# Performance work log

Hardware: AMD Instinct MI355X
Metric: run time of the kernel (lower is better)

The kernel has to match this reference:

```python
import jax, jax.numpy as jnp
import numpy as np

B, L, D, H, TOPK = 64, 1024, 16, 128, 64
SCALE = H ** -0.5  # proj_dim ** -0.5


def _linear_params(k, fan_in, fan_out):
    W = jax.random.normal(k, (fan_in, fan_out), jnp.float32) / np.sqrt(fan_in).astype(np.float32)
    b = jnp.zeros((fan_out,), jnp.float32)
    return W, b


def setup_inputs() -> dict:
    key = jax.random.key(0)
    ks = jax.random.split(key, 9)
    x = jax.random.normal(ks[0], (B, L, D), jnp.float32)
    Wq, bq = _linear_params(ks[1], D, H)
    Wk, bk = _linear_params(ks[2], D, H)
    phi_W1, phi_b1 = _linear_params(ks[3], D, H)
    phi_W2, phi_b2 = _linear_params(ks[4], H, H)
    xi_W1, xi_b1 = _linear_params(ks[5], 2 * D, H)
    xi_W2, xi_b2 = _linear_params(ks[6], H, H)
    rho_W1, rho_b1 = _linear_params(ks[7], H, H)
    rho_W2, rho_b2 = _linear_params(ks[8], H, H)
    return {
        "x": x,
        "Wq": Wq, "bq": bq, "Wk": Wk, "bk": bk,
        "phi_W1": phi_W1, "phi_b1": phi_b1, "phi_W2": phi_W2, "phi_b2": phi_b2,
        "xi_W1": xi_W1, "xi_b1": xi_b1, "xi_W2": xi_W2, "xi_b2": xi_b2,
        "rho_W1": rho_W1, "rho_b1": rho_b1, "rho_W2": rho_W2, "rho_b2": rho_b2,
    }


def _gather_rows(x, idx):
    # x: (B, L, D), idx: (B, K) -> (B, K, D)
    return jnp.take_along_axis(x, jnp.broadcast_to(idx[:, :, None], idx.shape + (x.shape[-1],)), axis=1)


def reference(x, Wq, bq, Wk, bk,
              phi_W1, phi_b1, phi_W2, phi_b2,
              xi_W1, xi_b1, xi_W2, xi_b2,
              rho_W1, rho_b1, rho_W2, rho_b2):
    # padding mask (trim is identity for dense random inputs; mask is all-True)
    mask = jnp.abs(x).sum(-1) != 0  # (B, L)
    Q = x @ Wq + bq                 # (B, L, H)
    K = x @ Wk + bk                 # (B, L, H)
    scores = jnp.einsum("blh,bmh->blm", Q, K) * SCALE  # (B, L, L)
    mask_2d = mask[:, :, None] & mask[:, None, :]
    scores = jnp.where(mask_2d, scores, -jnp.inf)
    flat = scores.reshape(B, L * L)
    topk_vals, topk_idx = jax.lax.top_k(flat, TOPK)    # (B, K)
    topk_w = jax.nn.softmax(topk_vals, axis=-1)
    row = topk_idx // L
    col = topk_idx % L
    x_i = _gather_rows(x, row)  # (B, K, D)
    x_j = _gather_rows(x, col)
    relu = jax.nn.relu
    feat_self = relu(x_i @ phi_W1 + phi_b1) @ phi_W2 + phi_b2
    pair = jnp.concatenate([x_i, x_j], axis=-1)
    feat_pair = relu(pair @ xi_W1 + xi_b1) @ xi_W2 + xi_b2
    self_mask = (row == col)[:, :, None]
    interaction = jnp.where(self_mask, feat_self, feat_pair)  # (B, K, H)
    pooled = jnp.sum(interaction * topk_w[:, :, None], axis=1)  # (B, H)
    return relu(pooled @ rho_W1 + rho_b1) @ rho_W2 + rho_b2
```

## Files before the change

### kernel.cpp

```cpp
#include <hip/hip_runtime.h>

typedef unsigned int uint;
typedef __attribute__((ext_vector_type(4))) float f4;

#define SCALEF 0.08838834764831845f
#define NBINS 4096
#define CAND_MAX 4096
#define SELC 1024
#define LLIST 512
#define T_LOOSE 3.3f

__device__ __forceinline__ uint ordmap(float v) {
  uint u = __float_as_uint(v);
  return (u & 0x80000000u) ? ~u : (u | 0x80000000u);
}

#define DOT4(a, b2) ((a).x*(b2).x + (a).y*(b2).y + (a).z*(b2).z + (a).w*(b2).w)

__global__ __launch_bounds__(256) void k_prep(const float* __restrict__ x,
    const float* __restrict__ Wq, const float* __restrict__ bq,
    const float* __restrict__ Wk, const float* __restrict__ bk,
    float* __restrict__ Gv, float* __restrict__ Hv,
    uint* __restrict__ ccnt, uint* __restrict__ ccnt2) {
  __shared__ float sWq[2048], sWk[2048];
  __shared__ float sA[256];
  __shared__ float su[16], sv[16], sc;
  int tid = threadIdx.x;
  int row = blockIdx.x * 256 + tid;
  if (blockIdx.x == 0 && tid < 128) { if (tid < 64) ccnt[tid] = 0; else ccnt2[tid - 64] = 0; }
  for (int i = tid; i < 512; i += 256) {
    ((float4*)sWq)[i] = ((const float4*)Wq)[i];
    ((float4*)sWk)[i] = ((const float4*)Wk)[i];
  }
  __syncthreads();
  {
    int d = tid >> 4, e = tid & 15;
    float s = 0.f;
#pragma unroll 8
    for (int h = 0; h < 128; h++) s += sWq[d * 128 + h] * sWk[e * 128 + h];
    sA[tid] = s * SCALEF;
  }
  if (tid < 16) {
    float s1 = 0.f, s2 = 0.f;
    for (int h = 0; h < 128; h++) { s1 += sWq[tid * 128 + h] * bk[h]; s2 += bq[h] * sWk[tid * 128 + h]; }
    su[tid] = s1 * SCALEF; sv[tid] = s2 * SCALEF;
  } else if (tid == 16) {
    float s = 0.f;
    for (int h = 0; h < 128; h++) s += bq[h] * bk[h];
    sc = s * SCALEF;
  }
  __syncthreads();
  float xr[16];
#pragma unroll
  for (int d = 0; d < 16; d += 4) *(float4*)&xr[d] = *(const float4*)&x[(size_t)row * 16 + d];
  float g[16];
#pragma unroll
  for (int e = 0; e < 16; e++) {
    float s = sv[e];
#pragma unroll
    for (int d = 0; d < 16; d++) s += xr[d] * sA[d * 16 + e];
    g[e] = s;
  }
  float hh = sc;
#pragma unroll
  for (int d = 0; d < 16; d++) hh += xr[d] * su[d];
#pragma unroll
  for (int e = 0; e < 16; e += 4) *(float4*)&Gv[(size_t)row * 16 + e] = *(float4*)&g[e];
  Hv[row] = hh;
}

__global__ __launch_bounds__(256, 4) void k_score(const float* __restrict__ Gv,
    const float* __restrict__ Hv, const float* __restrict__ x,
    uint* __restrict__ ccnt, int* __restrict__ cidx, float* __restrict__ cval) {
  int i = blockIdx.x;
  int b = i >> 5, t = i & 31, tm = t >> 3, tn = t & 7;
  __shared__ f4 sX4[512];
  __shared__ int lidx[LLIST];
  __shared__ float lval[LLIST];
  __shared__ uint lcnt, base_sh;
  int tid = threadIdx.x;
  if (tid == 0) lcnt = 0;
  const f4* xsrc = (const f4*)(x + ((size_t)b * 1024 + tn * 128) * 16);
  sX4[tid] = xsrc[tid];
  sX4[tid + 256] = xsrc[tid + 256];
  int lane = tid & 63, w = tid >> 6;
  const f4* gp = (const f4*)(Gv + ((size_t)b * 1024 + tm * 256 + lane) * 16);
  f4 gr[4][4];
  float hv[4];
#pragma unroll
  for (int k = 0; k < 4; k++) {
#pragma unroll
    for (int q = 0; q < 4; q++) gr[k][q] = gp[k * 256 + q];
    hv[k] = Hv[b * 1024 + tm * 256 + lane + 64 * k];
  }
  asm volatile("" : "+v"(gr[0][0]), "+v"(gr[0][1]), "+v"(gr[0][2]), "+v"(gr[0][3]),
                    "+v"(gr[1][0]), "+v"(gr[1][1]), "+v"(gr[1][2]), "+v"(gr[1][3]));
  asm volatile("" : "+v"(gr[2][0]), "+v"(gr[2][1]), "+v"(gr[2][2]), "+v"(gr[2][3]),
                    "+v"(gr[3][0]), "+v"(gr[3][1]), "+v"(gr[3][2]), "+v"(gr[3][3]));
  int r0g = tm * 256 + lane, c0g = tn * 128;
  __syncthreads();

#pragma unroll 2
  for (int cc = 0; cc < 32; ++cc) {
    int c = w * 32 + cc;
    f4 x0 = sX4[c * 4 + 0], x1 = sX4[c * 4 + 1];
    f4 x2 = sX4[c * 4 + 2], x3 = sX4[c * 4 + 3];
    float s[4];
#pragma unroll
    for (int k = 0; k < 4; k++)
      s[k] = (hv[k] + DOT4(gr[k][0], x0) + DOT4(gr[k][1], x1))
           + (DOT4(gr[k][2], x2) + DOT4(gr[k][3], x3));
#pragma unroll
    for (int k = 0; k < 4; k++) {
      if (__builtin_expect(s[k] >= T_LOOSE, 0)) {
        uint pos = atomicAdd(&lcnt, 1u);
        int fi = (r0g + 64 * k) * 1024 + (c0g + c);
        if (pos < LLIST) { lidx[pos] = fi; lval[pos] = s[k]; }
        else { uint gp2 = atomicAdd(&ccnt[b], 1u);
               if (gp2 < CAND_MAX) { cidx[b * CAND_MAX + gp2] = fi; cval[b * CAND_MAX + gp2] = s[k]; } }
      }
    }
  }
  __syncthreads();
  uint n = lcnt > LLIST ? LLIST : lcnt;
  if (tid == 0) base_sh = atomicAdd(&ccnt[b], n);
  __syncthreads();
  for (uint j = tid; j < n; j += 256) {
    uint p = base_sh + j;
    if (p < CAND_MAX) { cidx[b * CAND_MAX + p] = lidx[j]; cval[b * CAND_MAX + p] = lval[j]; }
  }
}

__device__ __forceinline__ void suffix_find(const uint* __restrict__ h1,
    uint* __restrict__ wtot, int tid, uint K,
    uint* __restrict__ bin_out, uint* __restrict__ above_out) {
  int lane = tid & 63, w = tid >> 6;
  uint s = h1[tid * 4] + h1[tid * 4 + 1] + h1[tid * 4 + 2] + h1[tid * 4 + 3];
  uint acc = s;
#pragma unroll
  for (int off = 1; off < 64; off <<= 1) {
    uint o = __shfl_down(acc, off);
    if (lane + off < 64) acc += o;
  }
  if (lane == 0) wtot[w] = acc;
  __syncthreads();
  uint wsuf = 0;
#pragma unroll
  for (int ww = 0; ww < 16; ww++) if (ww > w) wsuf += wtot[ww];
  uint suf_incl = acc + wsuf;
  uint suf_excl = suf_incl - s;
  if (suf_excl < K && suf_incl >= K) {
    uint run = suf_excl;
    for (int i2 = 3; i2 >= 0; i2--) {
      uint hv = h1[tid * 4 + i2];
      run += hv;
      if (run >= K) { *bin_out = (uint)(tid * 4 + i2); *above_out = run - hv; break; }
    }
  }
  __syncthreads();
}

__global__ __launch_bounds__(1024) void k_fallback(const float* __restrict__ Gv,
    const float* __restrict__ Hv, const float* __restrict__ x,
    const uint* __restrict__ ccnt, uint* __restrict__ ccnt2,
    int* __restrict__ cidx2, float* __restrict__ cval2) {
  int b = blockIdx.x;
  { uint c = ccnt[b]; if (c >= 64 && c <= CAND_MAX) return; }
  __shared__ uint h1[NBINS];
  __shared__ uint wtot[16];
  __shared__ uint bin_sh, above_sh;
  int tid = threadIdx.x;
  float xm[16];
#pragma unroll
  for (int d = 0; d < 16; d += 4) *(float4*)&xm[d] = *(const float4*)&x[((size_t)b * 1024 + tid) * 16 + d];
  for (int s2 = tid; s2 < NBINS; s2 += 1024) h1[s2] = 0;
  __syncthreads();
  for (int l = 0; l < 1024; l++) {
    float s = Hv[b * 1024 + l];
    const float* gl = Gv + ((size_t)b * 1024 + l) * 16;
#pragma unroll
    for (int d = 0; d < 16; d++) s += gl[d] * xm[d];
    atomicAdd(&h1[ordmap(s) >> 20], 1u);
  }
  __syncthreads();
  suffix_find(h1, wtot, tid, 64u, &bin_sh, &above_sh);
  uint B1 = bin_sh;
  uint need = 64u - above_sh;
  for (int s2 = tid; s2 < NBINS; s2 += 1024) h1[s2] = 0;
  __syncthreads();
  for (int l = 0; l < 1024; l++) {
    float s = Hv[b * 1024 + l];
    const float* gl = Gv + ((size_t)b * 1024 + l) * 16;
#pragma unroll
    for (int d = 0; d < 16; d++) s += gl[d] * xm[d];
    uint um = ordmap(s);
    if ((um >> 20) == B1) atomicAdd(&h1[(um >> 8) & 0xfffu], 1u);
  }
  __syncthreads();
  suffix_find(h1, wtot, tid, need, &bin_sh, &above_sh);
  uint P = (B1 << 12) | bin_sh;
  for (int l = 0; l < 1024; l++) {
    float s = Hv[b * 1024 + l];
    const float* gl = Gv + ((size_t)b * 1024 + l) * 16;
#pragma unroll
    for (int d = 0; d < 16; d++) s += gl[d] * xm[d];
    uint um = ordmap(s);
    if ((um >> 8) >= P) {
      uint pos = atomicAdd(&ccnt2[b], 1u);
      if (pos < CAND_MAX) { cidx2[b * CAND_MAX + pos] = l * 1024 + tid; cval2[b * CAND_MAX + pos] = s; }
    }
  }
}

__global__ __launch_bounds__(1024) void k_final(const float* __restrict__ x,
    const float* __restrict__ phiW1, const float* __restrict__ phib1,
    const float* __restrict__ phiW2, const float* __restrict__ phib2,
    const float* __restrict__ xiW1, const float* __restrict__ xib1,
    const float* __restrict__ xiW2, const float* __restrict__ xib2,
    const float* __restrict__ rhoW1, const float* __restrict__ rhob1,
    const float* __restrict__ rhoW2, const float* __restrict__ rhob2,
    const uint* __restrict__ ccnt, const int* __restrict__ cidx, const float* __restrict__ cval,
    const uint* __restrict__ ccnt2, const int* __restrict__ cidx2, const float* __restrict__ cval2,
    float* __restrict__ out) {
  int b = blockIdx.x;
  int tid = threadIdx.x;
  __shared__ float svals[CAND_MAX];
  __shared__ int   sidxs[CAND_MAX];
  __shared__ uint  h1[NBINS];
  __shared__ uint  wtot[16];
  __shared__ uint  bin_sh, above_sh;
  __shared__ float cv[SELC];
  __shared__ int   ci[SELC];
  __shared__ int   scnt_sh;
  __shared__ float sel_v[64], sel_w[64];
  __shared__ int   sel_l[64], sel_m[64];
  __shared__ float xpair[2048];
  __shared__ float psv[8][128], ppv[8][128];
  __shared__ float hsv[128], hpv[128];
  __shared__ float pacc[8][128];
  __shared__ float vec1[128], vec2[128];
  __shared__ float wsums[2];

  uint cmain = ccnt[b];
  int fl = (cmain < 64 || cmain > CAND_MAX) ? 1 : 0;
  const int*   clist = fl ? (cidx2 + (size_t)b * CAND_MAX) : (cidx + (size_t)b * CAND_MAX);
  const float* vlist = fl ? (cval2 + (size_t)b * CAND_MAX) : (cval + (size_t)b * CAND_MAX);
  uint craw = fl ? ccnt2[b] : cmain;
  int cnt = craw > CAND_MAX ? CAND_MAX : (int)craw;

  for (int j = tid; j < cnt; j += 1024) { svals[j] = vlist[j]; sidxs[j] = clist[j]; }
  for (int s = tid; s < NBINS; s += 1024) h1[s] = 0;
  if (tid == 0) scnt_sh = 0;
  if (tid < 64) { sel_v[tid] = -1e30f; sel_l[tid] = 0; sel_m[tid] = 0; }
  __syncthreads();

  for (int j = tid; j < cnt; j += 1024) atomicAdd(&h1[ordmap(svals[j]) >> 20], 1u);
  __syncthreads();
  suffix_find(h1, wtot, tid, 64u, &bin_sh, &above_sh);
  uint B1 = bin_sh;
  uint need = 64u - above_sh;
  for (int s = tid; s < NBINS; s += 1024) h1[s] = 0;
  __syncthreads();
  for (int j = tid; j < cnt; j += 1024) {
    uint um = ordmap(svals[j]);
    if ((um >> 20) == B1) atomicAdd(&h1[(um >> 8) & 0xfffu], 1u);
  }
  __syncthreads();
  suffix_find(h1, wtot, tid, need, &bin_sh, &above_sh);
  uint P = (B1 << 12) | bin_sh;

  for (int j = tid; j < cnt; j += 1024) {
    uint um = ordmap(svals[j]);
    if ((um >> 8) >= P) {
      int pos = atomicAdd(&scnt_sh, 1);
      if (pos < SELC) { cv[pos] = svals[j]; ci[pos] = sidxs[j]; }
    }
  }
  __syncthreads();
  int S = scnt_sh < SELC ? scnt_sh : SELC;

  for (int j = tid; j < S; j += 1024) {
    float vj = cv[j]; int ij = ci[j];
    int rank = 0;
    for (int i2 = 0; i2 < S; i2++) {
      float vi = cv[i2]; int ii = ci[i2];
      rank += (vi > vj || (vi == vj && ii < ij)) ? 1 : 0;
    }
    if (rank < 64) { sel_v[rank] = vj; sel_l[rank] = ij >> 10; sel_m[rank] = ij & 1023; }
  }
  __syncthreads();

  if (tid < 64) {
    float e = expf(sel_v[tid] - sel_v[0]);
    float ssum = e;
#pragma unroll
    for (int off = 1; off < 64; off <<= 1) ssum += __shfl_xor(ssum, off);
    float wj = e / ssum;
    sel_w[tid] = wj;
    int isself = (sel_l[tid] == sel_m[tid]) ? 1 : 0;
    float s0 = isself ? wj : 0.f, s1 = isself ? 0.f : wj;
#pragma unroll
    for (int off = 1; off < 64; off <<= 1) { s0 += __shfl_xor(s0, off); s1 += __shfl_xor(s1, off); }
    if (tid == 0) { wsums[0] = s0; wsums[1] = s1; }
  } else if (tid >= 512) {
    int t2 = tid - 512;
    int j = t2 >> 3, q = t2 & 7;
    int r = (q < 4) ? sel_l[j] : sel_m[j];
    ((float4*)xpair)[j * 8 + q] = *(const float4*)&x[((size_t)b * 1024 + r) * 16 + (q & 3) * 4];
  }
  __syncthreads();

  {
    int slice = tid >> 7, h = tid & 127;
    float wphi[16], wxi[32];
#pragma unroll
    for (int d = 0; d < 16; d++) wphi[d] = phiW1[d * 128 + h];
#pragma unroll
    for (int d = 0; d < 32; d++) wxi[d] = xiW1[d * 128 + h];
    float bphi = phib1[h], bxi = xib1[h];
    float accphi = 0.f, accxi = 0.f;
#pragma unroll
    for (int jj = 0; jj < 8; jj++) {
      int j = slice * 8 + jj;
      int l = sel_l[j], m = sel_m[j];
      float wj = sel_w[j];
      if (l == m) {
        float a = bphi;
#pragma unroll
        for (int d = 0; d < 16; d++) a += xpair[j * 32 + d] * wphi[d];
        accphi += wj * fmaxf(a, 0.f);
      } else {
        float a = bxi;
#pragma unroll
        for (int d = 0; d < 32; d++) a += xpair[j * 32 + d] * wxi[d];
        accxi += wj * fmaxf(a, 0.f);
      }
    }
    psv[slice][h] = accphi;
    ppv[slice][h] = accxi;
  }
  __syncthreads();
  if (tid < 256) {
    int hh = tid & 127;
    float s = 0.f;
    if (tid < 128) {
#pragma unroll
      for (int s2 = 0; s2 < 8; s2++) s += psv[s2][hh];
      hsv[hh] = s;
    } else {
#pragma unroll
      for (int s2 = 0; s2 < 8; s2++) s += ppv[s2][hh];
      hpv[hh] = s;
    }
  }
  __syncthreads();

  {
    int sl = tid >> 7, o = tid & 127;
    float p = 0.f;
#pragma unroll
    for (int hh2 = 0; hh2 < 16; hh2++) {
      int hh = sl * 16 + hh2;
      p += hsv[hh] * phiW2[hh * 128 + o] + hpv[hh] * xiW2[hh * 128 + o];
    }
    pacc[sl][o] = p;
  }
  __syncthreads();
  if (tid < 128) {
    float p = wsums[0] * phib2[tid] + wsums[1] * xib2[tid];
#pragma unroll
    for (int s2 = 0; s2 < 8; s2++) p += pacc[s2][tid];
    vec1[tid] = p;
  }
  __syncthreads();
  {
    int sl = tid >> 7, o = tid & 127;
    float p = 0.f;
#pragma unroll
    for (int hh2 = 0; hh2 < 16; hh2++) {
      int hh = sl * 16 + hh2;
      p += vec1[hh] * rhoW1[hh * 128 + o];
    }
    pacc[sl][o] = p;
  }
  __syncthreads();
  if (tid < 128) {
    float r = rhob1[tid];
#pragma unroll
    for (int s2 = 0; s2 < 8; s2++) r += pacc[s2][tid];
    vec2[tid] = fmaxf(r, 0.f);
  }
  __syncthreads();
  {
    int sl = tid >> 7, o = tid & 127;
    float p = 0.f;
#pragma unroll
    for (int hh2 = 0; hh2 < 16; hh2++) {
      int hh = sl * 16 + hh2;
      p += vec2[hh] * rhoW2[hh * 128 + o];
    }
    pacc[sl][o] = p;
  }
  __syncthreads();
  if (tid < 128) {
    float o2 = rhob2[tid];
#pragma unroll
    for (int s2 = 0; s2 < 8; s2++) o2 += pacc[s2][tid];
    out[(size_t)b * 128 + tid] = o2;
  }
}

extern "C" void kernel_launch(void* const* d_in, const int* in_sizes, int n_in,
                              void* d_out, int out_size, void* d_ws, size_t ws_size,
                              hipStream_t stream) {
  (void)in_sizes; (void)n_in; (void)out_size; (void)ws_size;
  const float* x     = (const float*)d_in[0];
  const float* Wq    = (const float*)d_in[1];
  const float* bq    = (const float*)d_in[2];
  const float* Wk    = (const float*)d_in[3];
  const float* bk    = (const float*)d_in[4];
  const float* phiW1 = (const float*)d_in[5];
  const float* phib1 = (const float*)d_in[6];
  const float* phiW2 = (const float*)d_in[7];
  const float* phib2 = (const float*)d_in[8];
  const float* xiW1  = (const float*)d_in[9];
  const float* xib1  = (const float*)d_in[10];
  const float* xiW2  = (const float*)d_in[11];
  const float* xib2  = (const float*)d_in[12];
  const float* rhoW1 = (const float*)d_in[13];
  const float* rhob1 = (const float*)d_in[14];
  const float* rhoW2 = (const float*)d_in[15];
  const float* rhob2 = (const float*)d_in[16];

  char* ws = (char*)d_ws;
  float* Gv   = (float*)(ws);
  float* Hv   = (float*)(ws + 4194304);
  uint*  ccnt = (uint*)(ws + 4456448);
  uint*  ccnt2= (uint*)(ws + 4456704);
  int*   cidx = (int*)(ws + 4457472);
  float* cval = (float*)(ws + 5506048);
  int*   cidx2= (int*)(ws + 6554624);
  float* cval2= (float*)(ws + 7603200);

  k_prep<<<256, 256, 0, stream>>>(x, Wq, bq, Wk, bk, Gv, Hv, ccnt, ccnt2);
  k_score<<<2048, 256, 0, stream>>>(Gv, Hv, x, ccnt, cidx, cval);
  k_fallback<<<64, 1024, 0, stream>>>(Gv, Hv, x, ccnt, ccnt2, cidx2, cval2);
  k_final<<<64, 1024, 0, stream>>>(x,
                                  phiW1, phib1, phiW2, phib2,
                                  xiW1, xib1, xiW2, xib2,
                                  rhoW1, rhob1, rhoW2, rhob2,
                                  ccnt, cidx, cval, ccnt2, cidx2, cval2,
                                  (float*)d_out);
}
```

Before: 162.5 us.

## Fold fallback top-k into final kernel, raise candidate threshold, use inline-asm loads

Removes the separate fallback kernel launch and moves the exact histogram-based fallback selection into k_final. Candidates now go straight into shared memory instead of a second global buffer. It raises the loose score threshold so fewer candidates are appended, which relies on at least 64 scores per batch exceeding it or else the slow in-block fallback runs. It also replaces the Gv register loads with explicit global_load_dwordx4 inline assembly and a single waitcnt, to batch the loads.

New measurement: 158.0 us. 2.7% less time.

```diff
diff --git a/kernel.cpp b/kernel.cpp
--- a/kernel.cpp
+++ b/kernel.cpp
@@ -8,7 +8,7 @@
 #define CAND_MAX 4096
 #define SELC 1024
 #define LLIST 512
-#define T_LOOSE 3.3f
+#define T_LOOSE 3.8f
 
 __device__ __forceinline__ uint ordmap(float v) {
   uint u = __float_as_uint(v);
@@ -20,14 +20,13 @@
 __global__ __launch_bounds__(256) void k_prep(const float* __restrict__ x,
     const float* __restrict__ Wq, const float* __restrict__ bq,
     const float* __restrict__ Wk, const float* __restrict__ bk,
-    float* __restrict__ Gv, float* __restrict__ Hv,
-    uint* __restrict__ ccnt, uint* __restrict__ ccnt2) {
+    float* __restrict__ Gv, float* __restrict__ Hv, uint* __restrict__ ccnt) {
   __shared__ float sWq[2048], sWk[2048];
   __shared__ float sA[256];
   __shared__ float su[16], sv[16], sc;
   int tid = threadIdx.x;
   int row = blockIdx.x * 256 + tid;
-  if (blockIdx.x == 0 && tid < 128) { if (tid < 64) ccnt[tid] = 0; else ccnt2[tid - 64] = 0; }
+  if (blockIdx.x == 0 && tid < 64) ccnt[tid] = 0;
   for (int i = tid; i < 512; i += 256) {
     ((float4*)sWq)[i] = ((const float4*)Wq)[i];
     ((float4*)sWk)[i] = ((const float4*)Wk)[i];
@@ -84,19 +83,21 @@
   sX4[tid] = xsrc[tid];
   sX4[tid + 256] = xsrc[tid + 256];
   int lane = tid & 63, w = tid >> 6;
-  const f4* gp = (const f4*)(Gv + ((size_t)b * 1024 + tm * 256 + lane) * 16);
+  const char* gbase = (const char*)(Gv + ((size_t)b * 1024 + tm * 256 + lane) * 16);
   f4 gr[4][4];
+#pragma unroll
+  for (int k = 0; k < 4; k++) {
+    const char* a = gbase + k * 4096;
+    asm volatile("global_load_dwordx4 %0, %1, off"           : "=&v"(gr[k][0]) : "v"(a));
+    asm volatile("global_load_dwordx4 %0, %1, off offset:16" : "=&v"(gr[k][1]) : "v"(a));
+    asm volatile("global_load_dwordx4 %0, %1, off offset:32" : "=&v"(gr[k][2]) : "v"(a));
+    asm volatile("global_load_dwordx4 %0, %1, off offset:48" : "=&v"(gr[k][3]) : "v"(a));
+  }
   float hv[4];
 #pragma unroll
-  for (int k = 0; k < 4; k++) {
-#pragma unroll
-    for (int q = 0; q < 4; q++) gr[k][q] = gp[k * 256 + q];
-    hv[k] = Hv[b * 1024 + tm * 256 + lane + 64 * k];
-  }
-  asm volatile("" : "+v"(gr[0][0]), "+v"(gr[0][1]), "+v"(gr[0][2]), "+v"(gr[0][3]),
-                    "+v"(gr[1][0]), "+v"(gr[1][1]), "+v"(gr[1][2]), "+v"(gr[1][3]));
-  asm volatile("" : "+v"(gr[2][0]), "+v"(gr[2][1]), "+v"(gr[2][2]), "+v"(gr[2][3]),
-                    "+v"(gr[3][0]), "+v"(gr[3][1]), "+v"(gr[3][2]), "+v"(gr[3][3]));
+  for (int k = 0; k < 4; k++) hv[k] = Hv[b * 1024 + tm * 256 + lane + 64 * k];
+  asm volatile("s_waitcnt vmcnt(0)" ::: "memory");
+  __builtin_amdgcn_sched_barrier(0);
   int r0g = tm * 256 + lane, c0g = tn * 128;
   __syncthreads();
 
@@ -160,59 +161,8 @@
   __syncthreads();
 }
 
-__global__ __launch_bounds__(1024) void k_fallback(const float* __restrict__ Gv,
-    const float* __restrict__ Hv, const float* __restrict__ x,
-    const uint* __restrict__ ccnt, uint* __restrict__ ccnt2,
-    int* __restrict__ cidx2, float* __restrict__ cval2) {
-  int b = blockIdx.x;
-  { uint c = ccnt[b]; if (c >= 64 && c <= CAND_MAX) return; }
-  __shared__ uint h1[NBINS];
-  __shared__ uint wtot[16];
-  __shared__ uint bin_sh, above_sh;
-  int tid = threadIdx.x;
-  float xm[16];
-#pragma unroll
-  for (int d = 0; d < 16; d += 4) *(float4*)&xm[d] = *(const float4*)&x[((size_t)b * 1024 + tid) * 16 + d];
-  for (int s2 = tid; s2 < NBINS; s2 += 1024) h1[s2] = 0;
-  __syncthreads();
-  for (int l = 0; l < 1024; l++) {
-    float s = Hv[b * 1024 + l];
-    const float* gl = Gv + ((size_t)b * 1024 + l) * 16;
-#pragma unroll
-    for (int d = 0; d < 16; d++) s += gl[d] * xm[d];
-    atomicAdd(&h1[ordmap(s) >> 20], 1u);
-  }
-  __syncthreads();
-  suffix_find(h1, wtot, tid, 64u, &bin_sh, &above_sh);
-  uint B1 = bin_sh;
-  uint need = 64u - above_sh;
-  for (int s2 = tid; s2 < NBINS; s2 += 1024) h1[s2] = 0;
-  __syncthreads();
-  for (int l = 0; l < 1024; l++) {
-    float s = Hv[b * 1024 + l];
-    const float* gl = Gv + ((size_t)b * 1024 + l) * 16;
-#pragma unroll
-    for (int d = 0; d < 16; d++) s += gl[d] * xm[d];
-    uint um = ordmap(s);
-    if ((um >> 20) == B1) atomicAdd(&h1[(um >> 8) & 0xfffu], 1u);
-  }
-  __syncthreads();
-  suffix_find(h1, wtot, tid, need, &bin_sh, &above_sh);
-  uint P = (B1 << 12) | bin_sh;
-  for (int l = 0; l < 1024; l++) {
-    float s = Hv[b * 1024 + l];
-    const float* gl = Gv + ((size_t)b * 1024 + l) * 16;
-#pragma unroll
-    for (int d = 0; d < 16; d++) s += gl[d] * xm[d];
-    uint um = ordmap(s);
-    if ((um >> 8) >= P) {
-      uint pos = atomicAdd(&ccnt2[b], 1u);
-      if (pos < CAND_MAX) { cidx2[b * CAND_MAX + pos] = l * 1024 + tid; cval2[b * CAND_MAX + pos] = s; }
-    }
-  }
-}
-
 __global__ __launch_bounds__(1024) void k_final(const float* __restrict__ x,
+    const float* __restrict__ Gv, const float* __restrict__ Hv,
     const float* __restrict__ phiW1, const float* __restrict__ phib1,
     const float* __restrict__ phiW2, const float* __restrict__ phib2,
     const float* __restrict__ xiW1, const float* __restrict__ xib1,
@@ -220,7 +170,6 @@
     const float* __restrict__ rhoW1, const float* __restrict__ rhob1,
     const float* __restrict__ rhoW2, const float* __restrict__ rhob2,
     const uint* __restrict__ ccnt, const int* __restrict__ cidx, const float* __restrict__ cval,
-    const uint* __restrict__ ccnt2, const int* __restrict__ cidx2, const float* __restrict__ cval2,
     float* __restrict__ out) {
   int b = blockIdx.x;
   int tid = threadIdx.x;
@@ -231,7 +180,7 @@
   __shared__ uint  bin_sh, above_sh;
   __shared__ float cv[SELC];
   __shared__ int   ci[SELC];
-  __shared__ int   scnt_sh;
+  __shared__ int   scnt_sh, fcnt_sh;
   __shared__ float sel_v[64], sel_w[64];
   __shared__ int   sel_l[64], sel_m[64];
   __shared__ float xpair[2048];
@@ -243,15 +192,61 @@
 
   uint cmain = ccnt[b];
   int fl = (cmain < 64 || cmain > CAND_MAX) ? 1 : 0;
-  const int*   clist = fl ? (cidx2 + (size_t)b * CAND_MAX) : (cidx + (size_t)b * CAND_MAX);
-  const float* vlist = fl ? (cval2 + (size_t)b * CAND_MAX) : (cval + (size_t)b * CAND_MAX);
-  uint craw = fl ? ccnt2[b] : cmain;
-  int cnt = craw > CAND_MAX ? CAND_MAX : (int)craw;
-
-  for (int j = tid; j < cnt; j += 1024) { svals[j] = vlist[j]; sidxs[j] = clist[j]; }
+  int cnt;
+  if (tid == 0) { scnt_sh = 0; fcnt_sh = 0; }
+  if (tid < 64) { sel_v[tid] = -1e30f; sel_l[tid] = 0; sel_m[tid] = 0; }
+
+  if (!fl) {
+    cnt = (int)cmain;
+    for (int j = tid; j < cnt; j += 1024) {
+      svals[j] = cval[(size_t)b * CAND_MAX + j];
+      sidxs[j] = cidx[(size_t)b * CAND_MAX + j];
+    }
+  } else {
+    float xm[16];
+#pragma unroll
+    for (int d = 0; d < 16; d += 4) *(float4*)&xm[d] = *(const float4*)&x[((size_t)b * 1024 + tid) * 16 + d];
+    for (int s2 = tid; s2 < NBINS; s2 += 1024) h1[s2] = 0;
+    __syncthreads();
+    for (int l = 0; l < 1024; l++) {
+      float s = Hv[b * 1024 + l];
+      const float* gl = Gv + ((size_t)b * 1024 + l) * 16;
+#pragma unroll
+      for (int d = 0; d < 16; d++) s += gl[d] * xm[d];
+      atomicAdd(&h1[ordmap(s) >> 20], 1u);
+    }
+    __syncthreads();
+    suffix_find(h1, wtot, tid, 64u, &bin_sh, &above_sh);
+    uint B1f = bin_sh;
+    uint needf = 64u - above_sh;
+    for (int s2 = tid; s2 < NBINS; s2 += 1024) h1[s2] = 0;
+    __syncthreads();
+    for (int l = 0; l < 1024; l++) {
+      float s = Hv[b * 1024 + l];
+      const float* gl = Gv + ((size_t)b * 1024 + l) * 16;
+#pragma unroll
+      for (int d = 0; d < 16; d++) s += gl[d] * xm[d];
+      uint um = ordmap(s);
+      if ((um >> 20) == B1f) atomicAdd(&h1[(um >> 8) & 0xfffu], 1u);
+    }
+    __syncthreads();
+    suffix_find(h1, wtot, tid, needf, &bin_sh, &above_sh);
+    uint Pf = (B1f << 12) | bin_sh;
+    for (int l = 0; l < 1024; l++) {
+      float s = Hv[b * 1024 + l];
+      const float* gl = Gv + ((size_t)b * 1024 + l) * 16;
+#pragma unroll
+      for (int d = 0; d < 16; d++) s += gl[d] * xm[d];
+      uint um = ordmap(s);
+      if ((um >> 8) >= Pf) {
+        int pos = atomicAdd(&fcnt_sh, 1);
+        if (pos < CAND_MAX) { svals[pos] = s; sidxs[pos] = l * 1024 + tid; }
+      }
+    }
+    __syncthreads();
+    cnt = fcnt_sh < CAND_MAX ? fcnt_sh : CAND_MAX;
+  }
   for (int s = tid; s < NBINS; s += 1024) h1[s] = 0;
-  if (tid == 0) scnt_sh = 0;
-  if (tid < 64) { sel_v[tid] = -1e30f; sel_l[tid] = 0; sel_m[tid] = 0; }
   __syncthreads();
 
   for (int j = tid; j < cnt; j += 1024) atomicAdd(&h1[ordmap(svals[j]) >> 20], 1u);
@@ -436,19 +431,15 @@
   float* Gv   = (float*)(ws);
   float* Hv   = (float*)(ws + 4194304);
   uint*  ccnt = (uint*)(ws + 4456448);
-  uint*  ccnt2= (uint*)(ws + 4456704);
   int*   cidx = (int*)(ws + 4457472);
   float* cval = (float*)(ws + 5506048);
-  int*   cidx2= (int*)(ws + 6554624);
-  float* cval2= (float*)(ws + 7603200);
-
-  k_prep<<<256, 256, 0, stream>>>(x, Wq, bq, Wk, bk, Gv, Hv, ccnt, ccnt2);
+
+  k_prep<<<256, 256, 0, stream>>>(x, Wq, bq, Wk, bk, Gv, Hv, ccnt);
   k_score<<<2048, 256, 0, stream>>>(Gv, Hv, x, ccnt, cidx, cval);
-  k_fallback<<<64, 1024, 0, stream>>>(Gv, Hv, x, ccnt, ccnt2, cidx2, cval2);
-  k_final<<<64, 1024, 0, stream>>>(x,
+  k_final<<<64, 1024, 0, stream>>>(x, Gv, Hv,
                                   phiW1, phib1, phiW2, phib2,
                                   xiW1, xib1, xiW2, xib2,
                                   rhoW1, rhob1, rhoW2, rhob2,
-                                  ccnt, cidx, cval, ccnt2, cidx2, cval2,
+                                  ccnt, cidx, cval,
                                   (float*)d_out);
 }
```
